# Kernel tuning notes

Hardware: AMD Instinct MI355X
Metric: run time of the kernel (lower is better)

## Reference

```python
import jax, jax.numpy as jnp
import numpy as np

C = 256
NH, NL, NP_ = 8, 3, 4
HD = C // NH
NLAYERS = 6


def sine_pos(H, W, num_feats=128, temperature=10000.0, eps=1e-6):
    # mmdet SinePositionalEncoding with normalize=True and an all-zero padding mask:
    # cumsum of ones -> (i+1), normalized by last element (H or W) * 2*pi.
    scale = 2.0 * np.pi
    y = (jnp.arange(1, H + 1, dtype=jnp.float32) / (H + eps)) * scale
    x = (jnp.arange(1, W + 1, dtype=jnp.float32) / (W + eps)) * scale
    d = jnp.arange(num_feats, dtype=jnp.float32)
    dim_t = temperature ** (2.0 * jnp.floor(d / 2.0) / num_feats)

    def interleave(p):  # p: (n, num_feats) -> sin on even dims, cos on odd dims, interleaved
        return jnp.stack([jnp.sin(p[:, 0::2]), jnp.cos(p[:, 1::2])], axis=-1).reshape(p.shape[0], -1)

    py = interleave(y[:, None] / dim_t)  # (H, num_feats)
    px = interleave(x[:, None] / dim_t)  # (W, num_feats)
    pos = jnp.concatenate([jnp.broadcast_to(py[:, None, :], (H, W, num_feats)),
                           jnp.broadcast_to(px[None, :, :], (H, W, num_feats))], axis=-1)
    return pos.reshape(H * W, 2 * num_feats)


def ref_points(H, W):
    # normalized pixel centers, (x, y) order, shape (H*W, 2)
    ry = (jnp.arange(H, dtype=jnp.float32) + 0.5) / H
    rx = (jnp.arange(W, dtype=jnp.float32) + 0.5) / W
    gy, gx = jnp.meshgrid(ry, rx, indexing='ij')
    return jnp.stack([gx.ravel(), gy.ravel()], axis=-1)


def ln(x, w, b, eps=1e-5):
    m = x.mean(-1, keepdims=True)
    v = x.var(-1, keepdims=True)
    return (x - m) / jnp.sqrt(v + eps) * w + b


def gnorm(x, w, b, groups=32, eps=1e-5):
    B, Ch, H, W = x.shape
    xg = x.reshape(B, groups, Ch // groups, H, W)
    m = xg.mean((2, 3, 4), keepdims=True)
    v = xg.var((2, 3, 4), keepdims=True)
    xg = (xg - m) / jnp.sqrt(v + eps)
    return xg.reshape(B, Ch, H, W) * w[None, :, None, None] + b[None, :, None, None]


def conv3x3(x, w):
    return jax.lax.conv_general_dilated(x, w, (1, 1), 'SAME',
                                        dimension_numbers=('NCHW', 'OIHW', 'NCHW'))


def ms_deform(value, shapes, loc, aw):
    # value (B,S,NH,HD); loc (B,L,NH,NL,NP,2) normalized [0,1]; aw (B,L,NH,NL,NP)
    # Matches F.grid_sample(..., align_corners=False, padding_mode='zeros').
    B, S, nH, hd = value.shape
    Lq, nP = loc.shape[1], loc.shape[4]
    out = jnp.zeros((B, Lq, nH, hd), value.dtype)
    start = 0
    for lvl, (H, W) in enumerate(shapes):
        v = value[:, start:start + H * W].transpose(0, 2, 1, 3)  # (B,nH,HW,hd)
        start += H * W
        l = loc[:, :, :, lvl]                 # (B,Lq,nH,nP,2)
        px = l[..., 0] * W - 0.5
        py = l[..., 1] * H - 0.5
        x0 = jnp.floor(px); y0 = jnp.floor(py)
        lx = px - x0; ly = py - y0
        x0i = x0.astype(jnp.int32); y0i = y0.astype(jnp.int32)

        def tw(w_):  # (B,Lq,nH,nP) -> (B,nH,Lq*nP,1)
            return w_.transpose(0, 2, 1, 3).reshape(B, nH, Lq * nP, 1)

        def gather(xi, yi):
            valid = ((xi >= 0) & (xi < W) & (yi >= 0) & (yi < H)).astype(value.dtype)
            idx = jnp.clip(yi, 0, H - 1) * W + jnp.clip(xi, 0, W - 1)
            idx = idx.transpose(0, 2, 1, 3).reshape(B, nH, Lq * nP)
            g = jnp.take_along_axis(v, idx[..., None], axis=2)  # (B,nH,Lq*nP,hd)
            return g * tw(valid)

        samp = (gather(x0i, y0i) * tw((1 - lx) * (1 - ly))
                + gather(x0i + 1, y0i) * tw(lx * (1 - ly))
                + gather(x0i, y0i + 1) * tw((1 - lx) * ly)
                + gather(x0i + 1, y0i + 1) * tw(lx * ly))
        samp = samp.reshape(B, nH, Lq, nP, hd)
        out = out + jnp.einsum('bqhp,bhqpd->bqhd', aw[:, :, :, lvl], samp)
    return out.reshape(B, Lq, nH * hd)


def _forward(feat0, feat1, feat2, in0_w, in0_b, in1_w, in1_b, in2_w, in2_b,
             off_w, off_b, aw_w, aw_b, vp_w, vp_b, op_w, op_b,
             n1_w, n1_b, ff1_w, ff1_b, ff2_w, ff2_b, n2_w, n2_b,
             fn_w, fn_b, lat_w, lat_b, out_w, gnw, gnb):
    feats = [feat0, feat1, feat2]
    in_ws = [in0_w, in1_w, in2_w]; in_bs = [in0_b, in1_b, in2_b]
    B = feat0.shape[0]
    mlvl = [jnp.einsum('oi,bihw->bohw', w, f) + b[None, :, None, None]
            for f, w, b in zip(feats, in_ws, in_bs)]
    shapes = [(f.shape[2], f.shape[3]) for f in mlvl]
    src = jnp.concatenate([f.reshape(B, C, -1).transpose(0, 2, 1) for f in mlvl], axis=1)  # (B,L,C)
    pos = jnp.concatenate([sine_pos(H, W) for (H, W) in shapes], axis=0)[None]  # (1,L,C)
    ref = jnp.concatenate([ref_points(H, W) for (H, W) in shapes], axis=0)      # (L,2)
    L = ref.shape[0]
    ref = jnp.broadcast_to(ref[None, :, None, :], (B, L, NL, 2))
    norm = jnp.array([[w_, h_] for (h_, w_) in shapes], dtype=src.dtype)  # (NL,2) = (W,H)
    for i in range(NLAYERS):
        q = src + pos
        off = (q @ off_w[i].T + off_b[i]).reshape(B, L, NH, NL, NP_, 2)
        aw = jax.nn.softmax((q @ aw_w[i].T + aw_b[i]).reshape(B, L, NH, NL * NP_), axis=-1)
        aw = aw.reshape(B, L, NH, NL, NP_)
        value = (src @ vp_w[i].T + vp_b[i]).reshape(B, L, NH, HD)
        loc = ref[:, :, None, :, None, :] + off / norm[None, None, None, :, None, :]
        attn = ms_deform(value, shapes, loc, aw) @ op_w[i].T + op_b[i]
        src = ln(src + attn, n1_w[i], n1_b[i])
        ff = jax.nn.relu(src @ ff1_w[i].T + ff1_b[i]) @ ff2_w[i].T + ff2_b[i]
        src = ln(src + ff, n2_w[i], n2_b[i])
    src = ln(src, fn_w, fn_b)
    mems, s = [], 0
    for (H, W) in shapes:
        mems.append(src[:, s:s + H * W].transpose(0, 2, 1).reshape(B, C, H, W))
        s += H * W
    mf = jnp.einsum('oi,bihw->bohw', lat_w, mems[0]) + lat_b[None, :, None, None]
    for i in range(3):
        mf = jax.nn.relu(gnorm(conv3x3(mf, out_w[i]), gnw[i], gnb[i]))
    return (mf, mems[0], mems[1], mems[2])


def setup_inputs():
    ks = iter(jax.random.split(jax.random.key(0), 64))

    def rn(shape, s=0.02):
        return jax.random.normal(next(ks), shape, dtype=jnp.float32) * s

    return dict(
        feat0=rn((1, 256, 64, 64), 1.0),
        feat1=rn((1, 512, 32, 32), 1.0),
        feat2=rn((1, 1024, 16, 16), 1.0),
        in0_w=rn((256, 256)), in0_b=rn((256,)),
        in1_w=rn((256, 512)), in1_b=rn((256,)),
        in2_w=rn((256, 1024)), in2_b=rn((256,)),
        off_w=rn((6, 192, 256), 0.002), off_b=rn((6, 192), 0.5),
        aw_w=rn((6, 96, 256)), aw_b=jnp.zeros((6, 96), jnp.float32),
        vp_w=rn((6, 256, 256)), vp_b=rn((6, 256)),
        op_w=rn((6, 256, 256)), op_b=rn((6, 256)),
        n1_w=jnp.ones((6, 256), jnp.float32), n1_b=jnp.zeros((6, 256), jnp.float32),
        ff1_w=rn((6, 1024, 256)), ff1_b=rn((6, 1024)),
        ff2_w=rn((6, 256, 1024)), ff2_b=rn((6, 256)),
        n2_w=jnp.ones((6, 256), jnp.float32), n2_b=jnp.zeros((6, 256), jnp.float32),
        fn_w=jnp.ones((256,), jnp.float32), fn_b=jnp.zeros((256,), jnp.float32),
        lat_w=rn((256, 256)), lat_b=rn((256,)),
        out_w=rn((3, 256, 256, 3, 3)),
        gnw=jnp.ones((3, 256), jnp.float32), gnb=jnp.zeros((3, 256), jnp.float32),
    )


def reference(feat0, feat1, feat2, in0_w, in0_b, in1_w, in1_b, in2_w, in2_b,
              off_w, off_b, aw_w, aw_b, vp_w, vp_b, op_w, op_b,
              n1_w, n1_b, ff1_w, ff1_b, ff2_w, ff2_b, n2_w, n2_b,
              fn_w, fn_b, lat_w, lat_b, out_w, gnw, gnb):
    return _forward(feat0, feat1, feat2, in0_w, in0_b, in1_w, in1_b, in2_w, in2_b,
                    off_w, off_b, aw_w, aw_b, vp_w, vp_b, op_w, op_b,
                    n1_w, n1_b, ff1_w, ff1_b, ff2_w, ff2_b, n2_w, n2_b,
                    fn_w, fn_b, lat_w, lat_b, out_w, gnw, gnb)
```

## Files before the change

kernel.cpp:

```cpp
#include <hip/hip_runtime.h>
#include <math.h>

#define LTOT 5376

typedef __attribute__((ext_vector_type(8))) __bf16 bf16x8;
typedef __attribute__((ext_vector_type(4))) float f32x4;
typedef __attribute__((ext_vector_type(8))) unsigned short us8;
typedef __attribute__((ext_vector_type(4))) unsigned short us4;

static __device__ __forceinline__ float4 ld4(const float* p) { return *(const float4*)p; }

static __device__ __forceinline__ unsigned short f2bf(float f) {
    unsigned int u = __float_as_uint(f);
    return (unsigned short)((u + 0x7fffu + ((u >> 16) & 1u)) >> 16);
}
static __device__ __forceinline__ float bf2f(unsigned short s) {
    return __uint_as_float(((unsigned int)s) << 16);
}

static __device__ __forceinline__ void gl16(const unsigned short* g, unsigned short* l) {
    __builtin_amdgcn_global_load_lds(
        (const __attribute__((address_space(1))) unsigned int*)g,
        (__attribute__((address_space(3))) unsigned int*)l, 16, 0, 0);
}

__device__ __forceinline__ void gemm_core(
    const unsigned short* __restrict__ A,
    const unsigned short* __restrict__ B,
    const float* __restrict__ bias,
    float* __restrict__ C1, unsigned short* __restrict__ C2,
    const float* __restrict__ posf, unsigned short* __restrict__ qb,
    unsigned short* As, unsigned short* Bs,
    int m0, int mo0, int n0, int N, int K, int omode, int relu)
{
    const int tid  = threadIdx.x;
    const int wave = tid >> 6;
    const int lane = tid & 63;
    const int wm   = (wave >> 1) * 32;
    const int wn   = (wave & 1) * 32;
    const int fr   = lane & 15;
    const int ko   = lane >> 4;

    const int q0 = tid, q1 = tid + 256;
    const int r0 = q0 >> 3, c0v = (q0 & 7) ^ (r0 & 7);
    const int r1 = q1 >> 3, c1v = (q1 & 7) ^ (r1 & 7);
    const unsigned short* a0 = A + (size_t)(m0 + r0) * K + (c0v << 3);
    const unsigned short* a1 = A + (size_t)(m0 + r1) * K + (c1v << 3);
    int bn0 = n0 + r0; if (bn0 > N - 1) bn0 = N - 1;
    int bn1 = n0 + r1; if (bn1 > N - 1) bn1 = N - 1;
    const unsigned short* b0 = B + (size_t)bn0 * K + (c0v << 3);
    const unsigned short* b1 = B + (size_t)bn1 * K + (c1v << 3);
    const int wb = wave << 9;

    f32x4 acc[2][2] = {};
    const int nt = K >> 6;

    auto stage = [&](int buf, int t) {
        const int kof = t << 6;
        gl16(a0 + kof, As + buf * 4096 + wb);
        gl16(a1 + kof, As + buf * 4096 + 2048 + wb);
        gl16(b0 + kof, Bs + buf * 4096 + wb);
        gl16(b1 + kof, Bs + buf * 4096 + 2048 + wb);
    };

    stage(0, 0);
    stage(1, 1);
    asm volatile("s_waitcnt vmcnt(4)" ::: "memory");
    __builtin_amdgcn_s_barrier();
    __builtin_amdgcn_sched_barrier(0);

    for (int t = 0; t < nt; t++) {
        if (t + 2 < nt) stage((t + 2) % 3, t + 2);
        const unsigned short* Ab = As + (t % 3) * 4096;
        const unsigned short* Bb = Bs + (t % 3) * 4096;
        #pragma unroll
        for (int sub = 0; sub < 2; sub++) {
            bf16x8 af[2], bfr[2];
            const int kk = (sub << 2) + ko;
            #pragma unroll
            for (int i = 0; i < 2; i++) {
                int r = wm + i * 16 + fr;
                af[i] = *(const bf16x8*)&Ab[(r << 6) + ((kk ^ (r & 7)) << 3)];
                int c = wn + i * 16 + fr;
                bfr[i] = *(const bf16x8*)&Bb[(c << 6) + ((kk ^ (c & 7)) << 3)];
            }
            #pragma unroll
            for (int i = 0; i < 2; i++)
                #pragma unroll
                for (int j = 0; j < 2; j++)
                    acc[i][j] = __builtin_amdgcn_mfma_f32_16x16x32_bf16(af[i], bfr[j], acc[i][j], 0, 0, 0);
        }
        if (t + 1 < nt) {
            if (t + 2 < nt) asm volatile("s_waitcnt vmcnt(4) lgkmcnt(0)" ::: "memory");
            else            asm volatile("s_waitcnt vmcnt(0) lgkmcnt(0)" ::: "memory");
            __builtin_amdgcn_s_barrier();
            __builtin_amdgcn_sched_barrier(0);
        }
    }

    #pragma unroll
    for (int j = 0; j < 2; j++) {
        int col = n0 + wn + j * 16 + fr;
        if (col >= N) continue;
        float cb = bias[col];
        #pragma unroll
        for (int i = 0; i < 2; i++) {
            #pragma unroll
            for (int r = 0; r < 4; r++) {
                int row = mo0 + wm + i * 16 + ko * 4 + r;
                float v = acc[i][j][r] + cb;
                if (relu) v = fmaxf(v, 0.f);
                size_t off = (size_t)row * N + col;
                if (omode == 0)      C1[off] = v;
                else if (omode == 1) C2[off] = f2bf(v);
                else if (omode == 2) { C1[off] = v; C2[off] = f2bf(v); }
                else { C1[off] = v; C2[off] = f2bf(v); qb[off] = f2bf(v + posf[off]); }
            }
        }
    }
}

__global__ __launch_bounds__(256) void bgemm_k(
    const unsigned short* __restrict__ A, const unsigned short* __restrict__ B,
    const float* __restrict__ bias, float* __restrict__ C1, unsigned short* __restrict__ C2,
    int N, int K, int omode, int relu)
{
    __shared__ unsigned short As[3 * 4096], Bs[3 * 4096];
    int m = blockIdx.y * 64;
    gemm_core(A, B, bias, C1, C2, nullptr, nullptr, As, Bs, m, m, blockIdx.x * 64, N, K, omode, relu);
}

__global__ __launch_bounds__(256) void oavp_k(
    const unsigned short* __restrict__ qbb, const unsigned short* __restrict__ woa,
    const float* __restrict__ boa, float* __restrict__ oab,
    const unsigned short* __restrict__ srcb, const unsigned short* __restrict__ wvp,
    const float* __restrict__ bvp, unsigned short* __restrict__ valb)
{
    __shared__ unsigned short As[3 * 4096], Bs[3 * 4096];
    const int bx = blockIdx.x;
    const int m = blockIdx.y * 64;
    if (bx < 5)
        gemm_core(qbb,  woa, boa, oab, nullptr, nullptr, nullptr, As, Bs, m, m, bx * 64, 288, 256, 0, 0);
    else
        gemm_core(srcb, wvp, bvp, nullptr, valb, nullptr, nullptr, As, Bs, m, m, (bx - 5) * 64, 256, 256, 1, 0);
}

__global__ __launch_bounds__(256) void inproj_k(
    const unsigned short* __restrict__ fT0, const unsigned short* __restrict__ w0, const float* __restrict__ b0,
    const unsigned short* __restrict__ fT1, const unsigned short* __restrict__ w1, const float* __restrict__ b1,
    const unsigned short* __restrict__ fT2, const unsigned short* __restrict__ w2, const float* __restrict__ b2,
    float* __restrict__ src, unsigned short* __restrict__ srcb,
    const float* __restrict__ posf, unsigned short* __restrict__ qbb)
{
    __shared__ unsigned short As[3 * 4096], Bs[3 * 4096];
    const int by = blockIdx.y;
    const int n0 = blockIdx.x * 64;
    if (by < 64)
        gemm_core(fT0, w0, b0, src, srcb, posf, qbb, As, Bs, by * 64, by * 64, n0, 256, 256, 3, 0);
    else if (by < 80)
        gemm_core(fT1, w1, b1, src, srcb, posf, qbb, As, Bs, (by - 64) * 64, 4096 + (by - 64) * 64, n0, 256, 512, 3, 0);
    else
        gemm_core(fT2, w2, b2, src, srcb, posf, qbb, As, Bs, (by - 80) * 64, 5120 + (by - 80) * 64, n0, 256, 1024, 3, 0);
}

__global__ void cvtall_k(const float* __restrict__ s0, const float* __restrict__ s1,
                         const float* __restrict__ s2, const float* __restrict__ s3,
                         const float* __restrict__ s4, const float* __restrict__ s5,
                         const float* __restrict__ s6, const float* __restrict__ s7,
                         unsigned short* __restrict__ d)
{
    int i = blockIdx.x * blockDim.x + threadIdx.x;
    if (i >= 1114112) return;
    const float* s; int off;
    if      (i <   98304) { s = s0; off = 0; }
    else if (i <  196608) { s = s1; off = 98304; }
    else if (i <  589824) { s = s2; off = 196608; }
    else if (i <  983040) { s = s3; off = 589824; }
    else if (i <  999424) { s = s4; off = 983040; }
    else if (i < 1032192) { s = s5; off = 999424; }
    else if (i < 1097728) { s = s6; off = 1032192; }
    else                  { s = s7; off = 1097728; }
    float4 v = ld4(&s[(size_t)(i - off) << 2]);
    us4 r = { f2bf(v.x), f2bf(v.y), f2bf(v.z), f2bf(v.w) };
    *(us4*)&d[(size_t)i << 2] = r;
}

__global__ void cvtT_k(const float* __restrict__ src, unsigned short* __restrict__ dst, int Ci, int P)
{
    __shared__ float t[32][33];
    int c0 = blockIdx.y * 32, p0 = blockIdx.x * 32;
    int x = threadIdx.x, y = threadIdx.y;
    for (int i = y; i < 32; i += 8)
        t[i][x] = src[(size_t)(c0 + i) * P + p0 + x];
    __syncthreads();
    for (int i = y; i < 32; i += 8)
        dst[(size_t)(p0 + i) * Ci + c0 + x] = f2bf(t[x][i]);
}

__global__ void pack_oa_k(const float* __restrict__ off_w, const float* __restrict__ off_b,
                          const float* __restrict__ aw_w,  const float* __restrict__ aw_b,
                          unsigned short* __restrict__ w_oa, float* __restrict__ b_oa)
{
    int idx = blockIdx.x * blockDim.x + threadIdx.x;
    if (idx >= 6 * 288 * 256) return;
    int i = idx / 73728;
    int r = idx - i * 73728;
    int n = r >> 8;
    int k = r & 255;
    float v = (n < 192) ? off_w[((size_t)i * 192 + n) * 256 + k]
                        : aw_w[((size_t)i * 96 + (n - 192)) * 256 + k];
    w_oa[idx] = f2bf(v);
    if (k == 0)
        b_oa[i * 288 + n] = (n < 192) ? off_b[i * 192 + n] : aw_b[i * 96 + (n - 192)];
}

__global__ void wconv_k(const float* __restrict__ out_w, unsigned short* __restrict__ wcb)
{
    int idx = blockIdx.x * blockDim.x + threadIdx.x;
    if (idx >= 3 * 589824) return;
    int c   = idx / 589824;
    int r   = idx - c * 589824;
    int icc = r / 73728;
    int r2  = r - icc * 73728;
    int oc  = r2 / 288;
    int r3  = r2 - oc * 288;
    int tap = r3 >> 5;
    int sl  = r3 & 31;
    int ic  = icc * 32 + (((sl >> 3) ^ ((oc >> 1) & 3)) << 3) + (sl & 7);
    wcb[idx] = f2bf(out_w[(((size_t)(c * 256 + oc)) * 256 + ic) * 9 + tap]);
}

__global__ void posenc_k(float* __restrict__ pos)
{
    int idx = blockIdx.x * blockDim.x + threadIdx.x;
    if (idx >= LTOT * 128) return;
    int l = idx >> 7;
    int pr = idx & 127;
    int half = pr >> 6;
    int j = pr & 63;
    int HW, sh, p;
    if (l < 4096)      { HW = 64; sh = 6; p = l; }
    else if (l < 5120) { HW = 32; sh = 5; p = l - 4096; }
    else               { HW = 16; sh = 4; p = l - 5120; }
    int y = p >> sh;
    int x = p & (HW - 1);
    float T = powf(10000.f, (float)j * (1.f / 64.f));
    float coord = (half == 0) ? (float)(y + 1) : (float)(x + 1);
    float v = coord / ((float)HW + 1e-6f) * 6.283185307179586f;
    float arg = v / T;
    size_t base = (size_t)l * 256 + half * 128 + (j << 1);
    pos[base]     = sinf(arg);
    pos[base + 1] = cosf(arg);
}

__global__ __launch_bounds__(256) void msdef_k(
    const unsigned short* __restrict__ valb, const float* __restrict__ oab,
    unsigned short* __restrict__ out)
{
    __shared__ float sw[8 * 288];
    const int tid = threadIdx.x;
    const int bl = blockIdx.x;
    #pragma unroll
    for (int id = tid; id < 576; id += 256)
        ((float4*)sw)[id] = ((const float4*)(oab + (size_t)bl * 2304))[id];
    __syncthreads();

    const int p = tid >> 5;
    const int t = tid & 31;
    const int l = bl * 8 + p;
    const int h = t >> 2;
    const int co = (t & 3) << 3;
    const float* mo = sw + p * 288;

    float aw_r[12];
    {
        const float* sc = mo + 192 + h * 12;
        float mx = -1e30f;
        #pragma unroll
        for (int j = 0; j < 12; j++) { aw_r[j] = sc[j]; mx = fmaxf(mx, aw_r[j]); }
        float su = 0.f;
        #pragma unroll
        for (int j = 0; j < 12; j++) { aw_r[j] = expf(aw_r[j] - mx); su += aw_r[j]; }
        float inv = 1.f / su;
        #pragma unroll
        for (int j = 0; j < 12; j++) aw_r[j] *= inv;
    }

    float rx, ry;
    {
        int HW, sh, q;
        if (l < 4096)      { HW = 64; sh = 6; q = l; }
        else if (l < 5120) { HW = 32; sh = 5; q = l - 4096; }
        else               { HW = 16; sh = 4; q = l - 5120; }
        int y = q >> sh;
        int x = q & (HW - 1);
        rx = (x + 0.5f) / (float)HW;
        ry = (y + 0.5f) / (float)HW;
    }

    const int starts[3] = {0, 4096, 5120};
    const int dims[3]   = {64, 32, 16};
    float acc[8] = {};
    #pragma unroll
    for (int s = 0; s < 3; s++) {
        const int D = dims[s];
        const int st = starts[s];
        #pragma unroll
        for (int pt = 0; pt < 4; pt++) {
            float a  = aw_r[(s << 2) + pt];
            float px = rx * D + mo[h * 24 + (s << 3) + (pt << 1)]     - 0.5f;
            float py = ry * D + mo[h * 24 + (s << 3) + (pt << 1) + 1] - 0.5f;
            float x0f = floorf(px), y0f = floorf(py);
            float lx = px - x0f, ly = py - y0f;
            int x0 = (int)x0f, y0 = (int)y0f;
            float w00 = a * (1.f - lx) * (1.f - ly);
            float w10 = a * lx * (1.f - ly);
            float w01 = a * (1.f - lx) * ly;
            float w11 = a * lx * ly;
            #pragma unroll
            for (int cy = 0; cy < 2; cy++) {
                int yi = y0 + cy;
                if (yi < 0 || yi >= D) continue;
                #pragma unroll
                for (int cx = 0; cx < 2; cx++) {
                    int xi = x0 + cx;
                    if (xi < 0 || xi >= D) continue;
                    float w = cy ? (cx ? w11 : w01) : (cx ? w10 : w00);
                    us8 v = *(const us8*)&valb[((size_t)(st + yi * D + xi) << 8) + (h << 5) + co];
                    #pragma unroll
                    for (int e = 0; e < 8; e++)
                        acc[e] = fmaf(w, bf2f(v[e]), acc[e]);
                }
            }
        }
    }
    us8 r;
    #pragma unroll
    for (int e = 0; e < 8; e++) r[e] = f2bf(acc[e]);
    *(us8*)&out[((size_t)l << 8) + (h << 5) + co] = r;
}

template<bool HAS_ADD, bool HAS_POS>
__global__ __launch_bounds__(256) void ln_k(float* __restrict__ src, const float* __restrict__ add,
                                            const float* __restrict__ w, const float* __restrict__ b,
                                            unsigned short* __restrict__ outb,
                                            const float* __restrict__ posf,
                                            unsigned short* __restrict__ qbout)
{
    int row = blockIdx.x * 4 + (threadIdx.x >> 6);
    int lane = threadIdx.x & 63;
    size_t base = (size_t)row * 256 + (lane << 2);
    float4 x = ld4(&src[base]);
    if (HAS_ADD) {
        float4 a = ld4(&add[base]);
        x.x += a.x; x.y += a.y; x.z += a.z; x.w += a.w;
    }
    float s = x.x + x.y + x.z + x.w;
    #pragma unroll
    for (int o = 32; o > 0; o >>= 1) s += __shfl_xor(s, o, 64);
    float m = s * (1.f / 256.f);
    float d0 = x.x - m, d1 = x.y - m, d2 = x.z - m, d3 = x.w - m;
    float v = d0 * d0 + d1 * d1 + d2 * d2 + d3 * d3;
    #pragma unroll
    for (int o = 32; o > 0; o >>= 1) v += __shfl_xor(v, o, 64);
    float rs = rsqrtf(v * (1.f / 256.f) + 1e-5f);
    float4 wv = ld4(&w[lane << 2]);
    float4 bv = ld4(&b[lane << 2]);
    float4 o4;
    o4.x = d0 * rs * wv.x + bv.x;
    o4.y = d1 * rs * wv.y + bv.y;
    o4.z = d2 * rs * wv.z + bv.z;
    o4.w = d3 * rs * wv.w + bv.w;
    *(float4*)&src[base] = o4;
    us4 r = { f2bf(o4.x), f2bf(o4.y), f2bf(o4.z), f2bf(o4.w) };
    *(us4*)&outb[base] = r;
    if (HAS_POS) {
        float4 p4 = ld4(&posf[base]);
        us4 q = { f2bf(o4.x + p4.x), f2bf(o4.y + p4.y), f2bf(o4.z + p4.z), f2bf(o4.w + p4.w) };
        *(us4*)&qbout[base] = q;
    }
}

__global__ void tr_k(const float* __restrict__ src, float* __restrict__ dst, int HW)
{
    __shared__ float t[32][33];
    int p0 = blockIdx.x * 32, c0 = blockIdx.y * 32;
    int x = threadIdx.x, y = threadIdx.y;
    for (int i = y; i < 32; i += 8)
        t[i][x] = src[(size_t)(p0 + i) * 256 + c0 + x];
    __syncthreads();
    for (int i = y; i < 32; i += 8)
        dst[(size_t)(c0 + i) * HW + p0 + x] = t[x][i];
}

__global__ __launch_bounds__(256) void conv3b_k(const unsigned short* __restrict__ inb,
                                                const unsigned short* __restrict__ wcb,
                                                float* __restrict__ out)
{
    __shared__ __align__(16) unsigned char smem[43776];
    unsigned short* sIn = (unsigned short*)smem;
    unsigned short* sW  = (unsigned short*)(smem + 6912);
    float* sO = (float*)smem;

    const int tid = threadIdx.x;
    const int mb = blockIdx.x;
    const int y0 = (mb >> 2) << 2;
    const int x0 = (mb & 3) << 4;
    const int oc0 = blockIdx.y << 6;
    const int wave = tid >> 6, lane = tid & 63;
    const int wm = (wave >> 1) * 32, wn = (wave & 1) * 32;
    const int fr = lane & 15, ko = lane >> 4;

    f32x4 acc[2][2] = {};

    for (int icc = 0; icc < 8; icc++) {
        __syncthreads();
        #pragma unroll
        for (int id = tid; id < 432; id += 256) {
            int pxi = id >> 2, ch = id & 3;
            int r = pxi / 18, s = pxi - r * 18;
            int gy = y0 - 1 + r, gx = x0 - 1 + s;
            us8 v = {};
            if (gy >= 0 && gy < 64 && gx >= 0 && gx < 64)
                v = *(const us8*)&inb[((size_t)(gy * 64 + gx) << 8) + (icc << 5) + (ch << 3)];
            *(us8*)&sIn[(pxi << 5) + ((ch ^ ((s >> 1) & 3)) << 3)] = v;
        }
        const unsigned short* wsrc = wcb + (((size_t)icc * 256 + oc0) * 9 << 5);
        #pragma unroll
        for (int id = tid; id < 2304; id += 256)
            *(us8*)&sW[id << 3] = *(const us8*)&wsrc[id << 3];
        __syncthreads();

        #pragma unroll
        for (int tap = 0; tap < 9; tap++) {
            const int ky = tap / 3, kx = tap - ky * 3;
            bf16x8 a[2], b[2];
            #pragma unroll
            for (int i = 0; i < 2; i++) {
                int px = wm + i * 16 + fr;
                int r = (px >> 4) + ky;
                int s = (px & 15) + kx;
                a[i] = *(const bf16x8*)&sIn[(((r * 18 + s)) << 5) + ((ko ^ ((s >> 1) & 3)) << 3)];
            }
            #pragma unroll
            for (int j = 0; j < 2; j++) {
                int oc = wn + j * 16 + fr;
                b[j] = *(const bf16x8*)&sW[(((oc * 9) + tap) << 5) + ((ko ^ ((oc >> 1) & 3)) << 3)];
            }
            #pragma unroll
            for (int i = 0; i < 2; i++)
                #pragma unroll
                for (int j = 0; j < 2; j++)
                    acc[i][j] = __builtin_amdgcn_mfma_f32_16x16x32_bf16(a[i], b[j], acc[i][j], 0, 0, 0);
        }
    }

    __syncthreads();
    #pragma unroll
    for (int i = 0; i < 2; i++)
        #pragma unroll
        for (int j = 0; j < 2; j++) {
            int oc = wn + j * 16 + fr;
            int pxb = wm + i * 16 + ko * 4;
            *(f32x4*)&sO[oc * 68 + pxb] = acc[i][j];
        }
    __syncthreads();
    {
        int oc_r = tid >> 2, yy = tid & 3;
        float* dst = &out[(size_t)(oc0 + oc_r) * 4096 + (y0 + yy) * 64 + x0];
        const float* srcl = &sO[oc_r * 68 + yy * 16];
        #pragma unroll
        for (int q = 0; q < 4; q++)
            *(float4*)&dst[q * 4] = *(const float4*)&srcl[q * 4];
    }
}

__global__ __launch_bounds__(256) void gnstats_k(const float* __restrict__ x, float* __restrict__ st)
{
    int g = blockIdx.x;
    const float* p = x + (size_t)g * 8 * 4096;
    float s = 0.f, ss = 0.f;
    for (int i = threadIdx.x * 4; i < 32768; i += 1024) {
        float4 v = ld4(&p[i]);
        s  += v.x + v.y + v.z + v.w;
        ss += v.x * v.x + v.y * v.y + v.z * v.z + v.w * v.w;
    }
    #pragma unroll
    for (int o = 32; o > 0; o >>= 1) {
        s  += __shfl_xor(s, o, 64);
        ss += __shfl_xor(ss, o, 64);
    }
    __shared__ float rs[4], rss[4];
    int wid = threadIdx.x >> 6;
    if ((threadIdx.x & 63) == 0) { rs[wid] = s; rss[wid] = ss; }
    __syncthreads();
    if (threadIdx.x == 0) {
        float S = rs[0] + rs[1] + rs[2] + rs[3];
        float SS = rss[0] + rss[1] + rss[2] + rss[3];
        float m = S * (1.f / 32768.f);
        float var = SS * (1.f / 32768.f) - m * m;
        st[g * 2] = m;
        st[g * 2 + 1] = rsqrtf(var + 1e-5f);
    }
}

__global__ void gnapply_b_k(const float* __restrict__ x, const float* __restrict__ st,
                            const float* __restrict__ w, const float* __restrict__ b,
                            unsigned short* __restrict__ o)
{
    int i = blockIdx.x * blockDim.x + threadIdx.x;
    if (i >= 262144) return;
    int c = i >> 10;
    int g = c >> 3;
    int px0 = (i & 1023) << 2;
    float m = st[g * 2], rs = st[g * 2 + 1];
    float sw = w[c], sb = b[c];
    float4 v = ld4(&x[(size_t)i << 2]);
    float r0 = fmaxf((v.x - m) * rs * sw + sb, 0.f);
    float r1 = fmaxf((v.y - m) * rs * sw + sb, 0.f);
    float r2 = fmaxf((v.z - m) * rs * sw + sb, 0.f);
    float r3 = fmaxf((v.w - m) * rs * sw + sb, 0.f);
    o[(size_t)(px0 + 0) * 256 + c] = f2bf(r0);
    o[(size_t)(px0 + 1) * 256 + c] = f2bf(r1);
    o[(size_t)(px0 + 2) * 256 + c] = f2bf(r2);
    o[(size_t)(px0 + 3) * 256 + c] = f2bf(r3);
}

__global__ void gnapply_f_k(const float* __restrict__ x, const float* __restrict__ st,
                            const float* __restrict__ w, const float* __restrict__ b,
                            float* __restrict__ o)
{
    int i = blockIdx.x * blockDim.x + threadIdx.x;
    if (i >= 262144) return;
    int c = i >> 10;
    int g = c >> 3;
    float m = st[g * 2], rs = st[g * 2 + 1];
    float sw = w[c], sb = b[c];
    float4 v = ld4(&x[(size_t)i << 2]);
    float4 r;
    r.x = fmaxf((v.x - m) * rs * sw + sb, 0.f);
    r.y = fmaxf((v.y - m) * rs * sw + sb, 0.f);
    r.z = fmaxf((v.z - m) * rs * sw + sb, 0.f);
    r.w = fmaxf((v.w - m) * rs * sw + sb, 0.f);
    *(float4*)&o[(size_t)i << 2] = r;
}

extern "C" void kernel_launch(void* const* d_in, const int* in_sizes, int n_in,
                              void* d_out, int out_size, void* d_ws, size_t ws_size,
                              hipStream_t stream)
{
    (void)in_sizes; (void)n_in; (void)out_size; (void)ws_size;
    const float* feat0 = (const float*)d_in[0];
    const float* feat1 = (const float*)d_in[1];
    const float* feat2 = (const float*)d_in[2];
    const float* in0_w = (const float*)d_in[3];
    const float* in0_b = (const float*)d_in[4];
    const float* in1_w = (const float*)d_in[5];
    const float* in1_b = (const float*)d_in[6];
    const float* in2_w = (const float*)d_in[7];
    const float* in2_b = (const float*)d_in[8];
    const float* off_w = (const float*)d_in[9];
    const float* off_b = (const float*)d_in[10];
    const float* aw_w  = (const float*)d_in[11];
    const float* aw_b  = (const float*)d_in[12];
    const float* vp_w  = (const float*)d_in[13];
    const float* vp_b  = (const float*)d_in[14];
    const float* op_w  = (const float*)d_in[15];
    const float* op_b  = (const float*)d_in[16];
    const float* n1_w  = (const float*)d_in[17];
    const float* n1_b  = (const float*)d_in[18];
    const float* ff1_w = (const float*)d_in[19];
    const float* ff1_b = (const float*)d_in[20];
    const float* ff2_w = (const float*)d_in[21];
    const float* ff2_b = (const float*)d_in[22];
    const float* n2_w  = (const float*)d_in[23];
    const float* n2_b  = (const float*)d_in[24];
    const float* fn_w  = (const float*)d_in[25];
    const float* fn_b  = (const float*)d_in[26];
    const float* lat_w = (const float*)d_in[27];
    const float* lat_b = (const float*)d_in[28];
    const float* out_w = (const float*)d_in[29];
    const float* gnw   = (const float*)d_in[30];
    const float* gnb   = (const float*)d_in[31];
    float* out = (float*)d_out;

    float* ws     = (float*)d_ws;
    float* src    = ws;
    float* pos    = src  + 1376256;
    float* tmp    = pos  + 1376256;
    float* valbuf = tmp  + 1376256;
    float* oab    = valbuf + 1376256;
    float* stats  = oab  + 1548288;
    float* boa    = stats + 64;
    float* pong   = pos;

    unsigned short* valb = (unsigned short*)valbuf;
    unsigned short* latb = (unsigned short*)(valbuf + 688128);

    unsigned short* ub = (unsigned short*)(boa + 1728);
    unsigned short* srcb  = ub; ub += 1376256;
    unsigned short* qbb   = ub; ub += 1376256;
    unsigned short* msdb  = ub; ub += 1376256;
    unsigned short* ffhb  = ub; ub += 5505024;
    unsigned short* w_oa  = ub; ub += 442368;
    unsigned short* w_vp  = ub; ub += 393216;
    unsigned short* w_op  = ub; ub += 393216;
    unsigned short* w_ff1 = ub; ub += 1572864;
    unsigned short* w_ff2 = ub; ub += 1572864;
    unsigned short* w_in0 = ub; ub += 65536;
    unsigned short* w_in1 = ub; ub += 131072;
    unsigned short* w_in2 = ub; ub += 262144;
    unsigned short* w_lat = ub; ub += 65536;
    unsigned short* wcb   = ub; ub += 1769472;

    unsigned short* fT0 = ffhb;
    unsigned short* fT1 = ffhb + 1048576;
    unsigned short* fT2 = ffhb + 1572864;
    unsigned short* pingb = qbb;

    pack_oa_k<<<1728, 256, 0, stream>>>(off_w, off_b, aw_w, aw_b, w_oa, boa);
    wconv_k<<<6912, 256, 0, stream>>>(out_w, wcb);
    cvtall_k<<<4352, 256, 0, stream>>>(vp_w, op_w, ff1_w, ff2_w, in0_w, in1_w, in2_w, lat_w, w_vp);
    cvtT_k<<<dim3(128, 8), dim3(32, 8), 0, stream>>>(feat0, fT0, 256, 4096);
    cvtT_k<<<dim3(32, 16), dim3(32, 8), 0, stream>>>(feat1, fT1, 512, 1024);
    cvtT_k<<<dim3(8, 32),  dim3(32, 8), 0, stream>>>(feat2, fT2, 1024, 256);
    posenc_k<<<2688, 256, 0, stream>>>(pos);

    inproj_k<<<dim3(4, 84), 256, 0, stream>>>(fT0, w_in0, in0_b, fT1, w_in1, in1_b,
                                              fT2, w_in2, in2_b, src, srcb, pos, qbb);

    for (int i = 0; i < 6; i++) {
        oavp_k<<<dim3(9, 84), 256, 0, stream>>>(qbb, w_oa + i*73728, boa + i*288, oab,
                                                srcb, w_vp + i*65536, vp_b + i*256, valb);
        msdef_k<<<672, 256, 0, stream>>>(valb, oab, msdb);
        bgemm_k<<<dim3(4, 84), 256, 0, stream>>>(msdb, w_op + i*65536, op_b + i*256, tmp, nullptr, 256, 256, 0, 0);
        ln_k<true,false><<<1344, 256, 0, stream>>>(src, tmp, n1_w + i*256, n1_b + i*256, srcb, nullptr, nullptr);
        bgemm_k<<<dim3(16, 84), 256, 0, stream>>>(srcb, w_ff1 + i*262144, ff1_b + i*1024, nullptr, ffhb, 1024, 256, 1, 1);
        bgemm_k<<<dim3(4, 84), 256, 0, stream>>>(ffhb, w_ff2 + i*262144, ff2_b + i*256, tmp, nullptr, 256, 1024, 0, 0);
        if (i < 5)
            ln_k<true,true><<<1344, 256, 0, stream>>>(src, tmp, n2_w + i*256, n2_b + i*256, srcb, pos, qbb);
        else
            ln_k<true,false><<<1344, 256, 0, stream>>>(src, tmp, n2_w + i*256, n2_b + i*256, srcb, nullptr, nullptr);
    }
    ln_k<false,false><<<1344, 256, 0, stream>>>(src, nullptr, fn_w, fn_b, srcb, nullptr, nullptr);

    tr_k<<<dim3(128,8), dim3(32,8), 0, stream>>>(src,           out + 1048576, 4096);
    tr_k<<<dim3(32,8),  dim3(32,8), 0, stream>>>(src + 1048576, out + 2097152, 1024);
    tr_k<<<dim3(8,8),   dim3(32,8), 0, stream>>>(src + 1310720, out + 2359296, 256);

    bgemm_k<<<dim3(4, 64), 256, 0, stream>>>(srcb, w_lat, lat_b, nullptr, latb, 256, 256, 1, 0);

    conv3b_k<<<dim3(64,4), 256, 0, stream>>>(latb, wcb, pong);
    gnstats_k<<<32, 256, 0, stream>>>(pong, stats);
    gnapply_b_k<<<1024, 256, 0, stream>>>(pong, stats, gnw, gnb, pingb);

    conv3b_k<<<dim3(64,4), 256, 0, stream>>>(pingb, wcb + 589824, pong);
    gnstats_k<<<32, 256, 0, stream>>>(pong, stats);
    gnapply_b_k<<<1024, 256, 0, stream>>>(pong, stats, gnw + 256, gnb + 256, pingb);

    conv3b_k<<<dim3(64,4), 256, 0, stream>>>(pingb, wcb + 1179648, pong);
    gnstats_k<<<32, 256, 0, stream>>>(pong, stats);
    gnapply_f_k<<<1024, 256, 0, stream>>>(pong, stats, gnw + 512, gnb + 512, out);
}
```

Baseline: 642.3 us.

## Fuse output-projection and FFN2 GEMMs with residual add and LayerNorm

Adds a gemmln_k kernel in which each block computes a full 32x256 output row tile, then adds bias and residual and applies LayerNorm in-register, using a cross-wave reduction through shared memory. It replaces the bgemm_k+ln_k pairs after the output projection and after FFN2, which removes the fp32 tmp round-trip and two launches per layer. In exchange the grid drops from 336 blocks to 168, which lowers parallelism, especially for the K=1024 FFN2 GEMM. The variance is also now computed as E[x^2]-m^2.

```diff
diff --git a/kernel.cpp b/kernel.cpp
--- a/kernel.cpp
+++ b/kernel.cpp
@@ -161,6 +161,127 @@
         gemm_core(fT1, w1, b1, src, srcb, posf, qbb, As, Bs, (by - 64) * 64, 4096 + (by - 64) * 64, n0, 256, 512, 3, 0);
     else
         gemm_core(fT2, w2, b2, src, srcb, posf, qbb, As, Bs, (by - 80) * 64, 5120 + (by - 80) * 64, n0, 256, 1024, 3, 0);
+}
+
+template<bool HAS_POS>
+__global__ __launch_bounds__(256) void gemmln_k(
+    const unsigned short* __restrict__ A, const unsigned short* __restrict__ B,
+    const float* __restrict__ bias,
+    float* __restrict__ srcf, unsigned short* __restrict__ srcb,
+    const float* __restrict__ lnw, const float* __restrict__ lnb,
+    const float* __restrict__ posf, unsigned short* __restrict__ qbb, int K)
+{
+    __shared__ __align__(16) unsigned short sst[3 * 9216];
+    __shared__ float red4[32][4][2];
+    const int tid  = threadIdx.x;
+    const int wave = tid >> 6;
+    const int lane = tid & 63;
+    const int fr   = lane & 15;
+    const int ko   = lane >> 4;
+    const int wn   = wave << 6;
+    const int m0   = blockIdx.x << 5;
+
+    const int qa = (wave << 6) + lane;
+    const unsigned short* gA = A + (size_t)(m0 + (qa & 31)) * K + ((qa >> 5) << 3);
+    const unsigned short* gB[4];
+    #pragma unroll
+    for (int rho = 0; rho < 4; rho++) {
+        int q2 = rho * 256 + (wave << 6) + lane;
+        gB[rho] = B + (size_t)(q2 & 255) * K + ((q2 >> 8) << 3);
+    }
+
+    auto stage = [&](int buf, int t) {
+        const int kof = t << 5;
+        unsigned short* st = sst + buf * 9216;
+        if (wave < 2) gl16(gA + kof, st + (wave << 9));
+        #pragma unroll
+        for (int rho = 0; rho < 4; rho++)
+            gl16(gB[rho] + kof, st + 1024 + rho * 2048 + (wave << 9));
+    };
+
+    f32x4 acc[2][4] = {};
+    const int nt = K >> 5;
+
+    stage(0, 0);
+    stage(1, 1);
+    if (wave < 2) asm volatile("s_waitcnt vmcnt(5) lgkmcnt(0)" ::: "memory");
+    else          asm volatile("s_waitcnt vmcnt(4) lgkmcnt(0)" ::: "memory");
+    __builtin_amdgcn_s_barrier();
+    __builtin_amdgcn_sched_barrier(0);
+
+    for (int t = 0; t < nt; t++) {
+        if (t + 2 < nt) stage((t + 2) % 3, t + 2);
+        const unsigned short* cb = sst + (t % 3) * 9216;
+        bf16x8 af[2], bf4[4];
+        #pragma unroll
+        for (int i = 0; i < 2; i++)
+            af[i] = *(const bf16x8*)&cb[((ko << 5) + (i << 4) + fr) << 3];
+        #pragma unroll
+        for (int j = 0; j < 4; j++)
+            bf4[j] = *(const bf16x8*)&cb[1024 + (((ko << 8) + wn + (j << 4) + fr) << 3)];
+        #pragma unroll
+        for (int i = 0; i < 2; i++)
+            #pragma unroll
+            for (int j = 0; j < 4; j++)
+                acc[i][j] = __builtin_amdgcn_mfma_f32_16x16x32_bf16(af[i], bf4[j], acc[i][j], 0, 0, 0);
+        if (t + 1 < nt) {
+            if (t + 2 < nt) {
+                if (wave < 2) asm volatile("s_waitcnt vmcnt(5) lgkmcnt(0)" ::: "memory");
+                else          asm volatile("s_waitcnt vmcnt(4) lgkmcnt(0)" ::: "memory");
+            } else {
+                asm volatile("s_waitcnt vmcnt(0) lgkmcnt(0)" ::: "memory");
+            }
+            __builtin_amdgcn_s_barrier();
+            __builtin_amdgcn_sched_barrier(0);
+        }
+    }
+
+    float xv[2][4][4];
+    #pragma unroll
+    for (int i = 0; i < 2; i++) {
+        #pragma unroll
+        for (int rr = 0; rr < 4; rr++) {
+            const int lr  = (i << 4) + (ko << 2) + rr;
+            const int row = m0 + lr;
+            float ps = 0.f, ps2 = 0.f;
+            #pragma unroll
+            for (int j = 0; j < 4; j++) {
+                int c = wn + (j << 4) + fr;
+                float v = acc[i][j][rr] + bias[c] + srcf[(size_t)row * 256 + c];
+                xv[i][j][rr] = v;
+                ps += v; ps2 += v * v;
+            }
+            #pragma unroll
+            for (int o = 1; o < 16; o <<= 1) {
+                ps  += __shfl_xor(ps,  o, 64);
+                ps2 += __shfl_xor(ps2, o, 64);
+            }
+            if (fr == 0) { red4[lr][wave][0] = ps; red4[lr][wave][1] = ps2; }
+        }
+    }
+    __syncthreads();
+    #pragma unroll
+    for (int i = 0; i < 2; i++) {
+        #pragma unroll
+        for (int rr = 0; rr < 4; rr++) {
+            const int lr  = (i << 4) + (ko << 2) + rr;
+            const int row = m0 + lr;
+            float S  = red4[lr][0][0] + red4[lr][1][0] + red4[lr][2][0] + red4[lr][3][0];
+            float S2 = red4[lr][0][1] + red4[lr][1][1] + red4[lr][2][1] + red4[lr][3][1];
+            float m   = S * (1.f / 256.f);
+            float var = S2 * (1.f / 256.f) - m * m;
+            float rstd = rsqrtf(var + 1e-5f);
+            #pragma unroll
+            for (int j = 0; j < 4; j++) {
+                int c = wn + (j << 4) + fr;
+                float o = (xv[i][j][rr] - m) * rstd * lnw[c] + lnb[c];
+                size_t off = (size_t)row * 256 + c;
+                srcf[off] = o;
+                srcb[off] = f2bf(o);
+                if (HAS_POS) qbb[off] = f2bf(o + posf[off]);
+            }
+        }
+    }
 }
 
 __global__ void cvtall_k(const float* __restrict__ s0, const float* __restrict__ s1,
@@ -340,21 +461,14 @@
     *(us8*)&out[((size_t)l << 8) + (h << 5) + co] = r;
 }
 
-template<bool HAS_ADD, bool HAS_POS>
-__global__ __launch_bounds__(256) void ln_k(float* __restrict__ src, const float* __restrict__ add,
+__global__ __launch_bounds__(256) void ln_k(float* __restrict__ src,
                                             const float* __restrict__ w, const float* __restrict__ b,
-                                            unsigned short* __restrict__ outb,
-                                            const float* __restrict__ posf,
-                                            unsigned short* __restrict__ qbout)
+                                            unsigned short* __restrict__ outb)
 {
     int row = blockIdx.x * 4 + (threadIdx.x >> 6);
     int lane = threadIdx.x & 63;
     size_t base = (size_t)row * 256 + (lane << 2);
     float4 x = ld4(&src[base]);
-    if (HAS_ADD) {
-        float4 a = ld4(&add[base]);
-        x.x += a.x; x.y += a.y; x.z += a.z; x.w += a.w;
-    }
     float s = x.x + x.y + x.z + x.w;
     #pragma unroll
     for (int o = 32; o > 0; o >>= 1) s += __shfl_xor(s, o, 64);
@@ -374,11 +488,6 @@
     *(float4*)&src[base] = o4;
     us4 r = { f2bf(o4.x), f2bf(o4.y), f2bf(o4.z), f2bf(o4.w) };
     *(us4*)&outb[base] = r;
-    if (HAS_POS) {
-        float4 p4 = ld4(&posf[base]);
-        us4 q = { f2bf(o4.x + p4.x), f2bf(o4.y + p4.y), f2bf(o4.z + p4.z), f2bf(o4.w + p4.w) };
-        *(us4*)&qbout[base] = q;
-    }
 }
 
 __global__ void tr_k(const float* __restrict__ src, float* __restrict__ dst, int HW)
@@ -633,16 +742,21 @@
         oavp_k<<<dim3(9, 84), 256, 0, stream>>>(qbb, w_oa + i*73728, boa + i*288, oab,
                                                 srcb, w_vp + i*65536, vp_b + i*256, valb);
         msdef_k<<<672, 256, 0, stream>>>(valb, oab, msdb);
-        bgemm_k<<<dim3(4, 84), 256, 0, stream>>>(msdb, w_op + i*65536, op_b + i*256, tmp, nullptr, 256, 256, 0, 0);
-        ln_k<true,false><<<1344, 256, 0, stream>>>(src, tmp, n1_w + i*256, n1_b + i*256, srcb, nullptr, nullptr);
-        bgemm_k<<<dim3(16, 84), 256, 0, stream>>>(srcb, w_ff1 + i*262144, ff1_b + i*1024, nullptr, ffhb, 1024, 256, 1, 1);
-        bgemm_k<<<dim3(4, 84), 256, 0, stream>>>(ffhb, w_ff2 + i*262144, ff2_b + i*256, tmp, nullptr, 256, 1024, 0, 0);
+        gemmln_k<false><<<168, 256, 0, stream>>>(msdb, w_op + i*65536, op_b + i*256,
+                                                 src, srcb, n1_w + i*256, n1_b + i*256,
+                                                 nullptr, nullptr, 256);
+        bgemm_k<<<dim3(16, 84), 256, 0, stream>>>(srcb, w_ff1 + i*262144, ff1_b + i*1024,
+                                                  nullptr, ffhb, 1024, 256, 1, 1);
         if (i < 5)
-            ln_k<true,true><<<1344, 256, 0, stream>>>(src, tmp, n2_w + i*256, n2_b + i*256, srcb, pos, qbb);
+            gemmln_k<true><<<168, 256, 0, stream>>>(ffhb, w_ff2 + i*262144, ff2_b + i*256,
+                                                    src, srcb, n2_w + i*256, n2_b + i*256,
+                                                    pos, qbb, 1024);
         else
-            ln_k<true,false><<<1344, 256, 0, stream>>>(src, tmp, n2_w + i*256, n2_b + i*256, srcb, nullptr, nullptr);
-    }
-    ln_k<false,false><<<1344, 256, 0, stream>>>(src, nullptr, fn_w, fn_b, srcb, nullptr, nullptr);
+            gemmln_k<false><<<168, 256, 0, stream>>>(ffhb, w_ff2 + i*262144, ff2_b + i*256,
+                                                     src, srcb, n2_w + i*256, n2_b + i*256,
+                                                     nullptr, nullptr, 1024);
+    }
+    ln_k<<<1344, 256, 0, stream>>>(src, fn_w, fn_b, srcb);
 
     tr_k<<<dim3(128,8), dim3(32,8), 0, stream>>>(src,           out + 1048576, 4096);
     tr_k<<<dim3(32,8),  dim3(32,8), 0, stream>>>(src + 1048576, out + 2097152, 1024);
```

Result: slower. 774.1 us (+20.5%).
